# Kernel tuning notes

Measured on AMD Instinct MI355X. Metric: run time of the kernel, lower is better.

Reference implementation:

```python
import jax, jax.numpy as jnp
import numpy as np

B, N, S = 8, 8192, 2048
IN, SKIP, OUT, EXP = 256, 128, 256, 4
GROUPS = 8


def conv1d(x, w, b):
    # 1x1 conv: x [B,C,N], w [O,C], b [O]
    return jnp.einsum('bcn,oc->bon', x, w) + b[None, :, None]


def group_norm(x, w, b, groups=GROUPS, eps=1e-5):
    Bb, C, Nn = x.shape
    xg = x.reshape(Bb, groups, C // groups, Nn)
    m = xg.mean(axis=(2, 3), keepdims=True)
    v = xg.var(axis=(2, 3), keepdims=True)
    xn = ((xg - m) * jax.lax.rsqrt(v + eps)).reshape(Bb, C, Nn)
    return xn * w[None, :, None] + b[None, :, None]


def _forward(xyz1, points1, xyz2, points2, t_emb, c_emb,
             mlp_w, mlp_b, mlp_gw, mlp_gb,
             c1w, c1b, g1w, g1b, c2w, c2b, g2w, g2b,
             tw, tb, cw, cb):
    # pairwise squared distances [B,N,S]
    dists = (-2.0 * jnp.einsum('bcn,bcm->bnm', xyz1, xyz2)
             + jnp.sum(xyz1 ** 2, axis=1)[:, :, None]
             + jnp.sum(xyz2 ** 2, axis=1)[:, None, :])
    neg_d3, idx = jax.lax.top_k(-dists, 3)          # 3 smallest distances
    d3 = -neg_d3                                     # [B,N,3]
    recip = 1.0 / (d3 + 1e-8)
    weight = recip / jnp.sum(recip, axis=2, keepdims=True)
    # gather neighbor features: points2 [B,C,S], idx [B,N,3] -> [B,C,N,3]
    gathered = jax.vmap(lambda p, i: p[:, i])(points2, idx)
    interp = jnp.sum(gathered * weight[:, None, :, :], axis=3)  # [B,IN,N]

    new_points = jnp.concatenate([points1, interp], axis=1)     # [B,IN+SKIP,N]
    x = jax.nn.silu(group_norm(conv1d(new_points, mlp_w, mlp_b), mlp_gw, mlp_gb))

    identity = x
    h = jax.nn.silu(group_norm(conv1d(x, c1w, c1b), g1w, g1b))
    h = group_norm(conv1d(h, c2w, c2b), g2w, g2b)
    st = t_emb @ tw.T + tb
    sc = c_emb @ cw.T + cb
    scale_t, shift_t = jnp.split(st, 2, axis=1)
    scale_c, shift_c = jnp.split(sc, 2, axis=1)
    scale = (scale_t + scale_c)[:, :, None]
    shift = (shift_t + shift_c)[:, :, None]
    h = h * (1.0 + scale) + shift
    return h + identity


def setup_inputs() -> dict:
    key = jax.random.key(0)
    ks = jax.random.split(key, 12)
    def rn(k, shape, s=1.0):
        return jax.random.normal(k, shape, dtype=jnp.float32) * s
    E = OUT * EXP
    return dict(
        xyz1=rn(ks[0], (B, 3, N)),
        points1=rn(ks[1], (B, SKIP, N)),
        xyz2=rn(ks[2], (B, 3, S)),
        points2=rn(ks[3], (B, IN, S)),
        t_emb=rn(ks[4], (B, OUT)),
        c_emb=rn(ks[5], (B, OUT)),
        mlp_w=rn(ks[6], (OUT, IN + SKIP), 0.02), mlp_b=jnp.zeros((OUT,), jnp.float32),
        mlp_gw=jnp.ones((OUT,), jnp.float32), mlp_gb=jnp.zeros((OUT,), jnp.float32),
        c1w=rn(ks[7], (E, OUT), 0.02), c1b=jnp.zeros((E,), jnp.float32),
        g1w=jnp.ones((E,), jnp.float32), g1b=jnp.zeros((E,), jnp.float32),
        c2w=rn(ks[8], (OUT, E), 0.02), c2b=jnp.zeros((OUT,), jnp.float32),
        g2w=jnp.ones((OUT,), jnp.float32), g2b=jnp.zeros((OUT,), jnp.float32),
        tw=rn(ks[9], (2 * OUT, OUT), 0.02), tb=jnp.zeros((2 * OUT,), jnp.float32),
        cw=rn(ks[10], (2 * OUT, OUT), 0.02), cb=jnp.zeros((2 * OUT,), jnp.float32),
    )


def reference(xyz1, points1, xyz2, points2, t_emb, c_emb,
              mlp_w, mlp_b, mlp_gw, mlp_gb,
              c1w, c1b, g1w, g1b, c2w, c2b, g2w, g2b,
              tw, tb, cw, cb):
    return _forward(xyz1, points1, xyz2, points2, t_emb, c_emb,
                    mlp_w, mlp_b, mlp_gw, mlp_gb,
                    c1w, c1b, g1w, g1b, c2w, c2b, g2w, g2b,
                    tw, tb, cw, cb)
```

## Files before the change

kernel.cpp:

```cpp
#include <hip/hip_runtime.h>
#include <hip/hip_bf16.h>

typedef unsigned short u16;
typedef __attribute__((ext_vector_type(4))) float f32x4;
typedef __attribute__((ext_vector_type(8))) short bf16x8;

typedef const __attribute__((address_space(1))) void GV;
typedef __attribute__((address_space(3))) void LV;
#define GLOAD16(g, l) __builtin_amdgcn_global_load_lds((GV*)(g), (LV*)(l), 16, 0, 0)

__device__ __forceinline__ float b2f(u16 u) {
    union { float f; unsigned int i; } v; v.i = ((unsigned int)u) << 16; return v.f;
}
__device__ __forceinline__ u16 f2b(float f) {
    union { float f; unsigned int i; } v; v.f = f;
    unsigned int x = v.i;
    return (u16)((x + 0x7fffu + ((x >> 16) & 1u)) >> 16);
}
__device__ __forceinline__ unsigned int cvt_pk_bf16(float lo, float hi) {
    unsigned int d;
    asm("v_cvt_pk_bf16_f32 %0, %1, %2" : "=v"(d) : "v"(lo), "v"(hi));
    return d;
}
__device__ __forceinline__ float silu(float t) {
    return t * __builtin_amdgcn_rcpf(1.f + __expf(-t));
}

__global__ void knn_part_kernel(const float* __restrict__ xyz1, const float* __restrict__ xyz2,
                                float2* __restrict__ cand) {
    __shared__ float4 spt[256];
    int b = blockIdx.z, ck = blockIdx.y, tid = threadIdx.x;
    const float* p2 = xyz2 + (size_t)b * 3 * 2048;
    int s0 = ck << 8;
    {
        int s = s0 + tid;
        float x = p2[s], y = p2[2048 + s], z = p2[4096 + s];
        spt[tid] = make_float4(x, y, z, (x * x + y * y) + z * z);
    }
    __syncthreads();
    int n = blockIdx.x * 256 + tid;
    const float* p1 = xyz1 + (size_t)b * 3 * 8192;
    float qx = p1[n], qy = p1[8192 + n], qz = p1[16384 + n];
    float qn = (qx * qx + qy * qy) + qz * qz;
    float d0 = 3.4e38f, d1 = 3.4e38f, d2 = 3.4e38f;
    int i0 = 0, i1 = 0, i2 = 0;
#pragma unroll 4
    for (int s = 0; s < 256; ++s) {
        float4 p = spt[s];
        float dot = (qx * p.x + qy * p.y) + qz * p.z;
        float d = (-2.f * dot + qn) + p.w;
        if (d < d2) {
            int gi = s0 + s;
            if (d < d1) {
                if (d < d0) { d2 = d1; i2 = i1; d1 = d0; i1 = i0; d0 = d; i0 = gi; }
                else        { d2 = d1; i2 = i1; d1 = d;  i1 = gi; }
            } else          { d2 = d;  i2 = gi; }
        }
    }
    float2* c = cand + (((size_t)b * 8192 + n) * 8 + ck) * 3;
    c[0] = make_float2(d0, __int_as_float(i0));
    c[1] = make_float2(d1, __int_as_float(i1));
    c[2] = make_float2(d2, __int_as_float(i2));
}

__global__ void knn_merge_kernel(const float2* __restrict__ cand,
                                 int* __restrict__ idx_out, float* __restrict__ w_out) {
    int t = blockIdx.x * 256 + threadIdx.x;
    const float2* c = cand + (size_t)t * 24;
    float d0 = 3.4e38f, d1 = 3.4e38f, d2 = 3.4e38f;
    int i0 = 0, i1 = 0, i2 = 0;
#pragma unroll
    for (int k = 0; k < 24; ++k) {
        float2 p = c[k];
        float d = p.x;
        if (d < d2) {
            int gi = __float_as_int(p.y);
            if (d < d1) {
                if (d < d0) { d2 = d1; i2 = i1; d1 = d0; i1 = i0; d0 = d; i0 = gi; }
                else        { d2 = d1; i2 = i1; d1 = d;  i1 = gi; }
            } else          { d2 = d;  i2 = gi; }
        }
    }
    float r0 = 1.f / (d0 + 1e-8f), r1 = 1.f / (d1 + 1e-8f), r2 = 1.f / (d2 + 1e-8f);
    float inv = 1.f / (r0 + r1 + r2);
    size_t base = (size_t)t * 3;
    idx_out[base] = i0; idx_out[base + 1] = i1; idx_out[base + 2] = i2;
    w_out[base] = r0 * inv; w_out[base + 1] = r1 * inv; w_out[base + 2] = r2 * inv;
}

__global__ void tr_kernel(const float* __restrict__ src, u16* __restrict__ dst,
                          int C, int S, int dstStride) {
    __shared__ u16 tile[64][70];
    int b = blockIdx.z;
    int s0 = blockIdx.x * 64, c0 = blockIdx.y * 64;
    int tid = threadIdx.x, lane = tid & 63, wv = tid >> 6;
    const float* sp = src + ((size_t)b * C + c0) * S + s0;
    for (int c = wv; c < 64; c += 4)
        tile[lane][c] = f2b(sp[(size_t)c * S + lane]);
    __syncthreads();
    u16* dp = dst + ((size_t)b * S + s0) * dstStride + c0;
    int s = tid >> 5, cp = tid & 31;
#pragma unroll
    for (int k = 0; k < 8; ++k) {
        int r = s + k * 8;
        unsigned int v = *(const unsigned int*)&tile[r][cp * 2];
        *(unsigned int*)&dp[(size_t)r * dstStride + cp * 2] = v;
    }
}

__global__ void build_x0_kernel(const u16* __restrict__ p2t,
                                const int* __restrict__ idx, const float* __restrict__ wgt,
                                u16* __restrict__ x0t) {
    int b = blockIdx.y;
    int n = blockIdx.x * 64 + (threadIdx.x >> 2);
    int q = threadIdx.x & 3;
    size_t ib = ((size_t)b * 8192 + n) * 3;
    int j0 = idx[ib], j1 = idx[ib + 1], j2 = idx[ib + 2];
    float w0 = wgt[ib], w1 = wgt[ib + 1], w2 = wgt[ib + 2];
    const u16* r0 = p2t + ((size_t)b * 2048 + j0) * 256;
    const u16* r1 = p2t + ((size_t)b * 2048 + j1) * 256;
    const u16* r2 = p2t + ((size_t)b * 2048 + j2) * 256;
    u16* out = x0t + ((size_t)b * 8192 + n) * 384;
#pragma unroll
    for (int i = 0; i < 8; ++i) {
        int c = (i * 4 + q) * 8;
        bf16x8 a0 = *(const bf16x8*)&r0[c];
        bf16x8 a1 = *(const bf16x8*)&r1[c];
        bf16x8 a2 = *(const bf16x8*)&r2[c];
        u16 ovu[8] __attribute__((aligned(16)));
#pragma unroll
        for (int j = 0; j < 8; ++j) {
            float v = w0 * b2f((u16)a0[j]) + w1 * b2f((u16)a1[j]) + w2 * b2f((u16)a2[j]);
            ovu[j] = f2b(v);
        }
        *(uint4*)&out[128 + c] = *(const uint4*)ovu;
    }
}

__global__ void cvt_kernel(const float* __restrict__ src, u16* __restrict__ dst, int n) {
    int i = blockIdx.x * 256 + threadIdx.x;
    if (i < n) dst[i] = f2b(src[i]);
}

__global__ void film_kernel(const float* __restrict__ t_emb, const float* __restrict__ c_emb,
                            const float* __restrict__ tw, const float* __restrict__ tb,
                            const float* __restrict__ cw, const float* __restrict__ cb,
                            float* __restrict__ film) {
    __shared__ float te[256], ce[256];
    int b = blockIdx.x, tid = threadIdx.x;
    te[tid] = t_emb[b * 256 + tid];
    ce[tid] = c_emb[b * 256 + tid];
    __syncthreads();
    int j = tid + blockIdx.y * 256;
    const float* twr = tw + (size_t)j * 256;
    const float* cwr = cw + (size_t)j * 256;
    float s = 0.f;
    for (int k = 0; k < 256; ++k) s += te[k] * twr[k] + ce[k] * cwr[k];
    s += tb[j] + cb[j];
    film[b * 512 + j] = s;
}

__global__ __launch_bounds__(512, 4) void gemm_kernel(
        const u16* __restrict__ At, const u16* __restrict__ W, const float* __restrict__ bias,
        u16* __restrict__ Out, float* __restrict__ part,
        int K, int M, int gshift) {
    __shared__ u16 lA[2][128 * 64];
    __shared__ u16 lB[2][128 * 64];
    __shared__ float bpart[4][2];
    int b = blockIdx.z;
    int n0 = blockIdx.x * 128, o0 = blockIdx.y * 128;
    int tid = threadIdx.x, lane = tid & 63, wv = tid >> 6;
    int wn = wv & 1, wo = wv >> 1;
    if (tid < 8) ((float*)bpart)[tid] = 0.f;
    f32x4 acc[4][2];
#pragma unroll
    for (int i = 0; i < 4; i++)
#pragma unroll
        for (int j = 0; j < 2; j++) acc[i][j] = (f32x4){0.f, 0.f, 0.f, 0.f};

    int rl = lane >> 3;
    int csw = ((lane & 7) ^ rl) * 8;
    const u16* aP[2];
    const u16* bP[2];
#pragma unroll
    for (int p2 = 0; p2 < 2; p2++) {
        int p = wv * 2 + p2;
        aP[p2] = At + ((size_t)b * 8192 + n0 + p * 8 + rl) * K + csw;
        bP[p2] = W + ((size_t)(o0 + p * 8 + rl)) * K + csw;
    }
    int nK = K >> 6;
#pragma unroll
    for (int p2 = 0; p2 < 2; p2++) {
        int p = wv * 2 + p2;
        GLOAD16(aP[p2], &lA[0][p * 512]);
        GLOAD16(bP[p2], &lB[0][p * 512]);
        aP[p2] += 64; bP[p2] += 64;
    }
    asm volatile("s_waitcnt vmcnt(0) lgkmcnt(0)" ::: "memory");
    __builtin_amdgcn_s_barrier();
    int cur = 0;
    for (int kt = 0; kt < nK; ++kt) {
        if (kt + 1 < nK) {
#pragma unroll
            for (int p2 = 0; p2 < 2; p2++) {
                int p = wv * 2 + p2;
                GLOAD16(aP[p2], &lA[cur ^ 1][p * 512]);
                GLOAD16(bP[p2], &lB[cur ^ 1][p * 512]);
                aP[p2] += 64; bP[p2] += 64;
            }
        }
        const u16* la = lA[cur];
        const u16* lb = lB[cur];
#pragma unroll
        for (int kk = 0; kk < 2; kk++) {
            bf16x8 af[4], bfr[2];
#pragma unroll
            for (int mf = 0; mf < 4; mf++) {
                int R = wn * 64 + mf * 16 + (lane & 15);
                af[mf] = *(const bf16x8*)&la[R * 64 + ((kk * 4 + (lane >> 4)) ^ (R & 7)) * 8];
            }
#pragma unroll
            for (int nf = 0; nf < 2; nf++) {
                int R = wo * 32 + nf * 16 + (lane & 15);
                bfr[nf] = *(const bf16x8*)&lb[R * 64 + ((kk * 4 + (lane >> 4)) ^ (R & 7)) * 8];
            }
#pragma unroll
            for (int mf = 0; mf < 4; mf++)
#pragma unroll
                for (int nf = 0; nf < 2; nf++)
                    acc[mf][nf] = __builtin_amdgcn_mfma_f32_16x16x32_bf16(bfr[nf], af[mf], acc[mf][nf], 0, 0, 0);
        }
        if (kt + 1 < nK)
            asm volatile("s_waitcnt vmcnt(0)" ::: "memory");
        __builtin_amdgcn_s_barrier();
        cur ^= 1;
    }
    int oq = (lane >> 4) * 4;
    float4 bs[2];
    float s1[2] = {0.f, 0.f}, s2[2] = {0.f, 0.f};
#pragma unroll
    for (int nf = 0; nf < 2; nf++) bs[nf] = *(const float4*)&bias[o0 + wo * 32 + nf * 16 + oq];
#pragma unroll
    for (int mf = 0; mf < 4; mf++) {
        int n = n0 + wn * 64 + mf * 16 + (lane & 15);
        u16* rowp = Out + ((size_t)b * 8192 + n) * M + o0 + wo * 32 + oq;
#pragma unroll
        for (int nf = 0; nf < 2; nf++) {
            float v0 = acc[mf][nf][0] + bs[nf].x;
            float v1 = acc[mf][nf][1] + bs[nf].y;
            float v2 = acc[mf][nf][2] + bs[nf].z;
            float v3 = acc[mf][nf][3] + bs[nf].w;
            s1[nf] += (v0 + v1) + (v2 + v3);
            s2[nf] += (v0 * v0 + v1 * v1) + (v2 * v2 + v3 * v3);
            uint2 pk;
            pk.x = cvt_pk_bf16(v0, v1);
            pk.y = cvt_pk_bf16(v2, v3);
            *(uint2*)&rowp[nf * 16] = pk;
        }
    }
#pragma unroll
    for (int nf = 0; nf < 2; nf++) {
        float a = s1[nf], c = s2[nf];
#pragma unroll
        for (int off = 32; off > 0; off >>= 1) {
            a += __shfl_xor(a, off, 64);
            c += __shfl_xor(c, off, 64);
        }
        if (lane == 0) {
            int gl = (wo * 32 + nf * 16) >> gshift;
            atomicAdd(&bpart[gl][0], a);
            atomicAdd(&bpart[gl][1], c);
        }
    }
    __syncthreads();
    int nlg = 128 >> gshift;
    if (tid < 2 * nlg) {
        int gl = tid >> 1, s = tid & 1;
        int g = (o0 >> gshift) + gl;
        part[(((size_t)b * 8 + g) * 2 + s) * 64 + blockIdx.x] = bpart[gl][s];
    }
}

__global__ __launch_bounds__(512, 4) void gemm_gn_kernel(
        const u16* __restrict__ At, const u16* __restrict__ W, const float* __restrict__ bias,
        const float* __restrict__ tab,
        u16* __restrict__ Out, float* __restrict__ part,
        int K, int M, int gshift) {
    __shared__ u16 lA[2][128 * 64];
    __shared__ u16 lB[2][128 * 64];
    __shared__ float cA[1024], cB[1024];
    __shared__ float bpart[4][2];
    int b = blockIdx.z;
    int n0 = blockIdx.x * 128, o0 = blockIdx.y * 128;
    int tid = threadIdx.x, lane = tid & 63, wv = tid >> 6;
    int wn = wv & 1, wo = wv >> 1;
    if (tid < 8) ((float*)bpart)[tid] = 0.f;
    f32x4 acc[4][2];
#pragma unroll
    for (int i = 0; i < 4; i++)
#pragma unroll
        for (int j = 0; j < 2; j++) acc[i][j] = (f32x4){0.f, 0.f, 0.f, 0.f};

    int rl = lane >> 3;
    int csw = ((lane & 7) ^ rl) * 8;
    const u16* aP[2];
    const u16* bP[2];
#pragma unroll
    for (int p2 = 0; p2 < 2; p2++) {
        int p = wv * 2 + p2;
        aP[p2] = At + ((size_t)b * 8192 + n0 + p * 8 + rl) * K + csw;
        bP[p2] = W + ((size_t)(o0 + p * 8 + rl)) * K + csw;
    }
    int nK = K >> 6;
    uint4 areg[2];
#pragma unroll
    for (int p2 = 0; p2 < 2; p2++) { areg[p2] = *(const uint4*)aP[p2]; aP[p2] += 64; }
#pragma unroll
    for (int p2 = 0; p2 < 2; p2++) {
        int p = wv * 2 + p2;
        GLOAD16(bP[p2], &lB[0][p * 512]);
        bP[p2] += 64;
    }
    {
        const float* tA = tab + (size_t)b * K;
        const float* tB = tab + (size_t)(8 + b) * K;
        for (int i = tid; i < K; i += 512) { cA[i] = tA[i]; cB[i] = tB[i]; }
    }
    __syncthreads();
#pragma unroll
    for (int p2 = 0; p2 < 2; p2++) {
        int p = wv * 2 + p2;
        int c = csw;
        const u16* rr = (const u16*)&areg[p2];
        float4 a0 = *(const float4*)&cA[c], a1 = *(const float4*)&cA[c + 4];
        float4 b0 = *(const float4*)&cB[c], b1 = *(const float4*)&cB[c + 4];
        float va[8] = {a0.x, a0.y, a0.z, a0.w, a1.x, a1.y, a1.z, a1.w};
        float vb[8] = {b0.x, b0.y, b0.z, b0.w, b1.x, b1.y, b1.z, b1.w};
        float v[8];
#pragma unroll
        for (int j = 0; j < 8; ++j) v[j] = silu(b2f(rr[j]) * va[j] + vb[j]);
        uint4 o;
        o.x = cvt_pk_bf16(v[0], v[1]); o.y = cvt_pk_bf16(v[2], v[3]);
        o.z = cvt_pk_bf16(v[4], v[5]); o.w = cvt_pk_bf16(v[6], v[7]);
        *(uint4*)&lA[0][p * 512 + lane * 8] = o;
    }
    asm volatile("s_waitcnt vmcnt(0) lgkmcnt(0)" ::: "memory");
    __builtin_amdgcn_s_barrier();
    int cur = 0;
    for (int kt = 0; kt < nK; ++kt) {
        if (kt + 1 < nK) {
#pragma unroll
            for (int p2 = 0; p2 < 2; p2++) { areg[p2] = *(const uint4*)aP[p2]; aP[p2] += 64; }
#pragma unroll
            for (int p2 = 0; p2 < 2; p2++) {
                int p = wv * 2 + p2;
                GLOAD16(bP[p2], &lB[cur ^ 1][p * 512]);
                bP[p2] += 64;
            }
        }
        const u16* la = lA[cur];
        const u16* lb = lB[cur];
#pragma unroll
        for (int kk = 0; kk < 2; kk++) {
            bf16x8 af[4], bfr[2];
#pragma unroll
            for (int mf = 0; mf < 4; mf++) {
                int R = wn * 64 + mf * 16 + (lane & 15);
                af[mf] = *(const bf16x8*)&la[R * 64 + ((kk * 4 + (lane >> 4)) ^ (R & 7)) * 8];
            }
#pragma unroll
            for (int nf = 0; nf < 2; nf++) {
                int R = wo * 32 + nf * 16 + (lane & 15);
                bfr[nf] = *(const bf16x8*)&lb[R * 64 + ((kk * 4 + (lane >> 4)) ^ (R & 7)) * 8];
            }
#pragma unroll
            for (int mf = 0; mf < 4; mf++)
#pragma unroll
                for (int nf = 0; nf < 2; nf++)
                    acc[mf][nf] = __builtin_amdgcn_mfma_f32_16x16x32_bf16(bfr[nf], af[mf], acc[mf][nf], 0, 0, 0);
        }
        if (kt + 1 < nK) {
            int c = (kt + 1) * 64 + csw;
            float4 a0 = *(const float4*)&cA[c], a1 = *(const float4*)&cA[c + 4];
            float4 b0 = *(const float4*)&cB[c], b1 = *(const float4*)&cB[c + 4];
            float va[8] = {a0.x, a0.y, a0.z, a0.w, a1.x, a1.y, a1.z, a1.w};
            float vb[8] = {b0.x, b0.y, b0.z, b0.w, b1.x, b1.y, b1.z, b1.w};
#pragma unroll
            for (int p2 = 0; p2 < 2; p2++) {
                int p = wv * 2 + p2;
                const u16* rr = (const u16*)&areg[p2];
                float v[8];
#pragma unroll
                for (int j = 0; j < 8; ++j) v[j] = silu(b2f(rr[j]) * va[j] + vb[j]);
                uint4 o;
                o.x = cvt_pk_bf16(v[0], v[1]); o.y = cvt_pk_bf16(v[2], v[3]);
                o.z = cvt_pk_bf16(v[4], v[5]); o.w = cvt_pk_bf16(v[6], v[7]);
                *(uint4*)&lA[cur ^ 1][p * 512 + lane * 8] = o;
            }
            asm volatile("s_waitcnt vmcnt(0)" ::: "memory");
        }
        asm volatile("s_waitcnt lgkmcnt(0)" ::: "memory");
        __builtin_amdgcn_s_barrier();
        cur ^= 1;
    }
    int oq = (lane >> 4) * 4;
    float4 bs[2];
    float s1[2] = {0.f, 0.f}, s2[2] = {0.f, 0.f};
#pragma unroll
    for (int nf = 0; nf < 2; nf++) bs[nf] = *(const float4*)&bias[o0 + wo * 32 + nf * 16 + oq];
#pragma unroll
    for (int mf = 0; mf < 4; mf++) {
        int n = n0 + wn * 64 + mf * 16 + (lane & 15);
        u16* rowp = Out + ((size_t)b * 8192 + n) * M + o0 + wo * 32 + oq;
#pragma unroll
        for (int nf = 0; nf < 2; nf++) {
            float v0 = acc[mf][nf][0] + bs[nf].x;
            float v1 = acc[mf][nf][1] + bs[nf].y;
            float v2 = acc[mf][nf][2] + bs[nf].z;
            float v3 = acc[mf][nf][3] + bs[nf].w;
            s1[nf] += (v0 + v1) + (v2 + v3);
            s2[nf] += (v0 * v0 + v1 * v1) + (v2 * v2 + v3 * v3);
            uint2 pk;
            pk.x = cvt_pk_bf16(v0, v1);
            pk.y = cvt_pk_bf16(v2, v3);
            *(uint2*)&rowp[nf * 16] = pk;
        }
    }
#pragma unroll
    for (int nf = 0; nf < 2; nf++) {
        float a = s1[nf], c = s2[nf];
#pragma unroll
        for (int off = 32; off > 0; off >>= 1) {
            a += __shfl_xor(a, off, 64);
            c += __shfl_xor(c, off, 64);
        }
        if (lane == 0) {
            int gl = (wo * 32 + nf * 16) >> gshift;
            atomicAdd(&bpart[gl][0], a);
            atomicAdd(&bpart[gl][1], c);
        }
    }
    __syncthreads();
    int nlg = 128 >> gshift;
    if (tid < 2 * nlg) {
        int gl = tid >> 1, s = tid & 1;
        int g = (o0 >> gshift) + gl;
        part[(((size_t)b * 8 + g) * 2 + s) * 64 + blockIdx.x] = bpart[gl][s];
    }
}

__global__ void gn_reduce_kernel(const float* __restrict__ part, float* __restrict__ stats) {
    int t = threadIdx.x;
    const float4* p = (const float4*)(part + (size_t)t * 64);
    float s = 0.f;
#pragma unroll
    for (int i = 0; i < 16; i++) { float4 v = p[i]; s += (v.x + v.y) + (v.z + v.w); }
    stats[t] = s;
}

__global__ void gn_coef_kernel(const float* __restrict__ stats, const float* __restrict__ gw,
                               const float* __restrict__ gb, float* __restrict__ tab,
                               int K, int gshift, float invCnt) {
    int c = blockIdx.x * 256 + threadIdx.x;
    int b = blockIdx.y;
    int g = c >> gshift;
    float sum = stats[(b * 8 + g) * 2], ssq = stats[(b * 8 + g) * 2 + 1];
    float m = sum * invCnt;
    float rstd = rsqrtf(fmaxf(ssq * invCnt - m * m, 0.f) + 1e-5f);
    float A = rstd * gw[c];
    tab[(size_t)b * K + c] = A;
    tab[(size_t)(8 + b) * K + c] = gb[c] - m * A;
}

__global__ void gn_apply_kernel(const u16* __restrict__ Yin, u16* __restrict__ Yout,
                                const float* __restrict__ tab) {
    int t = blockIdx.x * 256 + threadIdx.x;
    int c8 = t & 31, c0 = c8 << 3;
    int row0 = t >> 5;
    int rowstep = (gridDim.x * 256) >> 5;
    float A[8], Bc[8];
    int bprev = -1;
    for (int row = row0; row < 65536; row += rowstep) {
        int b = row >> 13;
        if (b != bprev) {
            bprev = b;
            float4 a0 = *(const float4*)(tab + (size_t)b * 256 + c0);
            float4 a1 = *(const float4*)(tab + (size_t)b * 256 + c0 + 4);
            float4 b0 = *(const float4*)(tab + (size_t)(8 + b) * 256 + c0);
            float4 b1 = *(const float4*)(tab + (size_t)(8 + b) * 256 + c0 + 4);
            A[0]=a0.x;A[1]=a0.y;A[2]=a0.z;A[3]=a0.w;A[4]=a1.x;A[5]=a1.y;A[6]=a1.z;A[7]=a1.w;
            Bc[0]=b0.x;Bc[1]=b0.y;Bc[2]=b0.z;Bc[3]=b0.w;Bc[4]=b1.x;Bc[5]=b1.y;Bc[6]=b1.z;Bc[7]=b1.w;
        }
        size_t off = ((size_t)row << 8) + c0;
        uint4 v4 = *(const uint4*)(Yin + off);
        const u16* vu = (const u16*)&v4;
        float v[8];
#pragma unroll
        for (int j = 0; j < 8; j++) v[j] = silu(b2f(vu[j]) * A[j] + Bc[j]);
        uint4 o;
        o.x = cvt_pk_bf16(v[0], v[1]); o.y = cvt_pk_bf16(v[2], v[3]);
        o.z = cvt_pk_bf16(v[4], v[5]); o.w = cvt_pk_bf16(v[6], v[7]);
        *(uint4*)(Yout + off) = o;
    }
}

__global__ void final_kernel(const u16* __restrict__ Y2, const u16* __restrict__ Xraw,
                             const float* __restrict__ g0w, const float* __restrict__ g0b,
                             const float* __restrict__ stats0,
                             const float* __restrict__ g2w, const float* __restrict__ g2b,
                             const float* __restrict__ stats2, const float* __restrict__ film,
                             float* __restrict__ out) {
    __shared__ float tile[64][257];
    int b = blockIdx.y, n0 = blockIdx.x * 64, tid = threadIdx.x;
    const float invCnt = 1.f / (32.f * 8192.f);
    int c8 = tid & 31, c0 = c8 << 3, g = c8 >> 2;
    float sum = stats2[(b * 8 + g) * 2], ssq = stats2[(b * 8 + g) * 2 + 1];
    float m = sum * invCnt, rstd = rsqrtf(fmaxf(ssq * invCnt - m * m, 0.f) + 1e-5f);
    float sum0 = stats0[(b * 8 + g) * 2], ssq0 = stats0[(b * 8 + g) * 2 + 1];
    float m0 = sum0 * invCnt, rstd0 = rsqrtf(fmaxf(ssq0 * invCnt - m0 * m0, 0.f) + 1e-5f);
    float4 w0 = *(const float4*)(g2w + c0), w1 = *(const float4*)(g2w + c0 + 4);
    float4 q0 = *(const float4*)(g2b + c0), q1 = *(const float4*)(g2b + c0 + 4);
    float4 f0 = *(const float4*)(film + b * 512 + c0), f1 = *(const float4*)(film + b * 512 + c0 + 4);
    float4 h0 = *(const float4*)(film + b * 512 + 256 + c0), h1 = *(const float4*)(film + b * 512 + 256 + c0 + 4);
    float4 u0 = *(const float4*)(g0w + c0), u1 = *(const float4*)(g0w + c0 + 4);
    float4 e0 = *(const float4*)(g0b + c0), e1 = *(const float4*)(g0b + c0 + 4);
    float wv[8] = {w0.x, w0.y, w0.z, w0.w, w1.x, w1.y, w1.z, w1.w};
    float qv[8] = {q0.x, q0.y, q0.z, q0.w, q1.x, q1.y, q1.z, q1.w};
    float fs[8] = {f0.x, f0.y, f0.z, f0.w, f1.x, f1.y, f1.z, f1.w};
    float fh[8] = {h0.x, h0.y, h0.z, h0.w, h1.x, h1.y, h1.z, h1.w};
    float uv[8] = {u0.x, u0.y, u0.z, u0.w, u1.x, u1.y, u1.z, u1.w};
    float ev[8] = {e0.x, e0.y, e0.z, e0.w, e1.x, e1.y, e1.z, e1.w};
    float A[8], Bc[8], A0[8], B0[8];
#pragma unroll
    for (int j = 0; j < 8; j++) {
        float sc = 1.f + fs[j];
        A[j] = rstd * wv[j] * sc;
        Bc[j] = (qv[j] - m * rstd * wv[j]) * sc + fh[j];
        A0[j] = rstd0 * uv[j];
        B0[j] = ev[j] - m0 * A0[j];
    }
    int nrb = tid >> 5;
#pragma unroll
    for (int k = 0; k < 8; k++) {
        int nr = nrb + k * 8;
        size_t base = ((size_t)b * 8192 + n0 + nr) * 256 + c0;
        uint4 yv = *(const uint4*)(Y2 + base);
        uint4 xv = *(const uint4*)(Xraw + base);
        const u16* yy = (const u16*)&yv;
        const u16* xx = (const u16*)&xv;
#pragma unroll
        for (int j = 0; j < 8; j++) {
            float x = silu(b2f(xx[j]) * A0[j] + B0[j]);
            tile[nr][c0 + j] = b2f(yy[j]) * A[j] + Bc[j] + x;
        }
    }
    __syncthreads();
    for (int q = tid; q < 256 * 16; q += 256) {
        int c = q >> 4, n4 = q & 15;
        float4 o;
        o.x = tile[n4 * 4 + 0][c];
        o.y = tile[n4 * 4 + 1][c];
        o.z = tile[n4 * 4 + 2][c];
        o.w = tile[n4 * 4 + 3][c];
        *(float4*)&out[((size_t)b * 256 + c) * 8192 + n0 + n4 * 4] = o;
    }
}

extern "C" void kernel_launch(void* const* d_in, const int* in_sizes, int n_in,
                              void* d_out, int out_size, void* d_ws, size_t ws_size,
                              hipStream_t stream) {
    const float* xyz1    = (const float*)d_in[0];
    const float* points1 = (const float*)d_in[1];
    const float* xyz2    = (const float*)d_in[2];
    const float* points2 = (const float*)d_in[3];
    const float* t_emb   = (const float*)d_in[4];
    const float* c_emb   = (const float*)d_in[5];
    const float* mlp_w   = (const float*)d_in[6];
    const float* mlp_b   = (const float*)d_in[7];
    const float* mlp_gw  = (const float*)d_in[8];
    const float* mlp_gb  = (const float*)d_in[9];
    const float* c1w     = (const float*)d_in[10];
    const float* c1b     = (const float*)d_in[11];
    const float* g1w     = (const float*)d_in[12];
    const float* g1b     = (const float*)d_in[13];
    const float* c2w     = (const float*)d_in[14];
    const float* c2b     = (const float*)d_in[15];
    const float* g2w     = (const float*)d_in[16];
    const float* g2b     = (const float*)d_in[17];
    const float* tw      = (const float*)d_in[18];
    const float* tb      = (const float*)d_in[19];
    const float* cw      = (const float*)d_in[20];
    const float* cb      = (const float*)d_in[21];

    char* ws = (char*)d_ws;
    int*   idx    = (int*)ws;
    float* wgt    = (float*)(ws + 786432);
    float* stats0 = (float*)(ws + 1572864);
    float* stats1 = (float*)(ws + 1573376);
    float* stats2 = (float*)(ws + 1573888);
    float* film   = (float*)(ws + 1574400);
    float* part0  = (float*)(ws + 1590784);
    float* part1  = (float*)(ws + 1623552);
    float* part2  = (float*)(ws + 1656320);
    u16* wb_mlp   = (u16*)(ws + 1689088);
    u16* wb_c1    = (u16*)(ws + 1885696);
    u16* wb_c2    = (u16*)(ws + 2409984);
    float* tab0   = (float*)(ws + 2934272);
    float* tab1   = (float*)(ws + 2950656);
    u16* X0t = (u16*)(ws + 4194304);
    u16* Y1t = (u16*)(ws + 54525952);
    u16* H1t = (u16*)(ws + 88080384);
    u16* Y2t = X0t;
    u16* Y1act = X0t;
    float2* cand = (float2*)X0t;
    u16* p2t = H1t;
    float* out = (float*)d_out;

    cvt_kernel<<<384, 256, 0, stream>>>(mlp_w, wb_mlp, 98304);
    cvt_kernel<<<1024, 256, 0, stream>>>(c1w, wb_c1, 262144);
    cvt_kernel<<<1024, 256, 0, stream>>>(c2w, wb_c2, 262144);
    knn_part_kernel<<<dim3(32, 8, 8), 256, 0, stream>>>(xyz1, xyz2, cand);
    knn_merge_kernel<<<256, 256, 0, stream>>>(cand, idx, wgt);
    tr_kernel<<<dim3(128, 2, 8), 256, 0, stream>>>(points1, X0t, 128, 8192, 384);
    tr_kernel<<<dim3(32, 4, 8), 256, 0, stream>>>(points2, p2t, 256, 2048, 256);
    build_x0_kernel<<<dim3(128, 8), 256, 0, stream>>>(p2t, idx, wgt, X0t);
    film_kernel<<<dim3(8, 2), 256, 0, stream>>>(t_emb, c_emb, tw, tb, cw, cb, film);
    gemm_kernel<<<dim3(64, 2, 8), 512, 0, stream>>>(X0t, wb_mlp, mlp_b, Y1t, part0, 384, 256, 5);
    gn_reduce_kernel<<<1, 128, 0, stream>>>(part0, stats0);
    gn_coef_kernel<<<dim3(1, 8), 256, 0, stream>>>(stats0, mlp_gw, mlp_gb, tab0, 256, 5, 1.f / (32.f * 8192.f));
    gn_apply_kernel<<<512, 256, 0, stream>>>(Y1t, Y1act, tab0);
    gemm_kernel<<<dim3(64, 8, 8), 512, 0, stream>>>(Y1act, wb_c1, c1b, H1t, part1, 256, 1024, 7);
    gn_reduce_kernel<<<1, 128, 0, stream>>>(part1, stats1);
    gn_coef_kernel<<<dim3(4, 8), 256, 0, stream>>>(stats1, g1w, g1b, tab1, 1024, 7, 1.f / (128.f * 8192.f));
    gemm_gn_kernel<<<dim3(64, 2, 8), 512, 0, stream>>>(H1t, wb_c2, c2b, tab1, Y2t, part2, 1024, 256, 5);
    gn_reduce_kernel<<<1, 128, 0, stream>>>(part2, stats2);
    final_kernel<<<dim3(128, 8), 256, 0, stream>>>(Y2t, Y1t, mlp_gw, mlp_gb, stats0,
                                                   g2w, g2b, stats2, film, out);
}
```

Measured before the change: 360.0 us.

## Halve GEMM K-tile to 32, fuse weight conversions and GN stats/coef kernels

```diff
diff --git a/kernel.cpp b/kernel.cpp
--- a/kernel.cpp
+++ b/kernel.cpp
@@ -137,9 +137,13 @@
     }
 }
 
-__global__ void cvt_kernel(const float* __restrict__ src, u16* __restrict__ dst, int n) {
+__global__ void cvt3_kernel(const float* __restrict__ s0, u16* __restrict__ d0, int n0,
+                            const float* __restrict__ s1, u16* __restrict__ d1, int n1,
+                            const float* __restrict__ s2, u16* __restrict__ d2, int n2) {
     int i = blockIdx.x * 256 + threadIdx.x;
-    if (i < n) dst[i] = f2b(src[i]);
+    if (i < n0) d0[i] = f2b(s0[i]);
+    if (i < n1) d1[i] = f2b(s1[i]);
+    if (i < n2) d2[i] = f2b(s2[i]);
 }
 
 __global__ void film_kernel(const float* __restrict__ t_emb, const float* __restrict__ c_emb,
@@ -164,8 +168,8 @@
         const u16* __restrict__ At, const u16* __restrict__ W, const float* __restrict__ bias,
         u16* __restrict__ Out, float* __restrict__ part,
         int K, int M, int gshift) {
-    __shared__ u16 lA[2][128 * 64];
-    __shared__ u16 lB[2][128 * 64];
+    __shared__ u16 lA[2][128 * 32];
+    __shared__ u16 lB[2][128 * 32];
     __shared__ float bpart[4][2];
     int b = blockIdx.z;
     int n0 = blockIdx.x * 128, o0 = blockIdx.y * 128;
@@ -178,58 +182,42 @@
 #pragma unroll
         for (int j = 0; j < 2; j++) acc[i][j] = (f32x4){0.f, 0.f, 0.f, 0.f};
 
-    int rl = lane >> 3;
-    int csw = ((lane & 7) ^ rl) * 8;
-    const u16* aP[2];
-    const u16* bP[2];
-#pragma unroll
-    for (int p2 = 0; p2 < 2; p2++) {
-        int p = wv * 2 + p2;
-        aP[p2] = At + ((size_t)b * 8192 + n0 + p * 8 + rl) * K + csw;
-        bP[p2] = W + ((size_t)(o0 + p * 8 + rl)) * K + csw;
-    }
-    int nK = K >> 6;
-#pragma unroll
-    for (int p2 = 0; p2 < 2; p2++) {
-        int p = wv * 2 + p2;
-        GLOAD16(aP[p2], &lA[0][p * 512]);
-        GLOAD16(bP[p2], &lB[0][p * 512]);
-        aP[p2] += 64; bP[p2] += 64;
-    }
+    int row = tid >> 2;
+    int csrc = ((tid & 3) ^ ((row >> 1) & 3)) * 8;
+    const u16* aP = At + ((size_t)b * 8192 + n0 + row) * K + csrc;
+    const u16* bP = W + ((size_t)(o0 + row)) * K + csrc;
+    int nK = K >> 5;
+    GLOAD16(aP, &lA[0][wv * 512]);
+    GLOAD16(bP, &lB[0][wv * 512]);
+    aP += 32; bP += 32;
     asm volatile("s_waitcnt vmcnt(0) lgkmcnt(0)" ::: "memory");
     __builtin_amdgcn_s_barrier();
     int cur = 0;
+    int cs = lane >> 4;
     for (int kt = 0; kt < nK; ++kt) {
         if (kt + 1 < nK) {
-#pragma unroll
-            for (int p2 = 0; p2 < 2; p2++) {
-                int p = wv * 2 + p2;
-                GLOAD16(aP[p2], &lA[cur ^ 1][p * 512]);
-                GLOAD16(bP[p2], &lB[cur ^ 1][p * 512]);
-                aP[p2] += 64; bP[p2] += 64;
-            }
+            GLOAD16(aP, &lA[cur ^ 1][wv * 512]);
+            GLOAD16(bP, &lB[cur ^ 1][wv * 512]);
+            aP += 32; bP += 32;
         }
         const u16* la = lA[cur];
         const u16* lb = lB[cur];
-#pragma unroll
-        for (int kk = 0; kk < 2; kk++) {
-            bf16x8 af[4], bfr[2];
-#pragma unroll
-            for (int mf = 0; mf < 4; mf++) {
-                int R = wn * 64 + mf * 16 + (lane & 15);
-                af[mf] = *(const bf16x8*)&la[R * 64 + ((kk * 4 + (lane >> 4)) ^ (R & 7)) * 8];
-            }
-#pragma unroll
-            for (int nf = 0; nf < 2; nf++) {
-                int R = wo * 32 + nf * 16 + (lane & 15);
-                bfr[nf] = *(const bf16x8*)&lb[R * 64 + ((kk * 4 + (lane >> 4)) ^ (R & 7)) * 8];
-            }
-#pragma unroll
-            for (int mf = 0; mf < 4; mf++)
-#pragma unroll
-                for (int nf = 0; nf < 2; nf++)
-                    acc[mf][nf] = __builtin_amdgcn_mfma_f32_16x16x32_bf16(bfr[nf], af[mf], acc[mf][nf], 0, 0, 0);
-        }
+        bf16x8 af[4], bfr[2];
+#pragma unroll
+        for (int mf = 0; mf < 4; mf++) {
+            int R = wn * 64 + mf * 16 + (lane & 15);
+            af[mf] = *(const bf16x8*)&la[R * 32 + ((cs ^ ((R >> 1) & 3)) * 8)];
+        }
+#pragma unroll
+        for (int nf = 0; nf < 2; nf++) {
+            int R = wo * 32 + nf * 16 + (lane & 15);
+            bfr[nf] = *(const bf16x8*)&lb[R * 32 + ((cs ^ ((R >> 1) & 3)) * 8)];
+        }
+#pragma unroll
+        for (int mf = 0; mf < 4; mf++)
+#pragma unroll
+            for (int nf = 0; nf < 2; nf++)
+                acc[mf][nf] = __builtin_amdgcn_mfma_f32_16x16x32_bf16(bfr[nf], af[mf], acc[mf][nf], 0, 0, 0);
         if (kt + 1 < nK)
             asm volatile("s_waitcnt vmcnt(0)" ::: "memory");
         __builtin_amdgcn_s_barrier();
@@ -286,8 +274,8 @@
         const float* __restrict__ tab,
         u16* __restrict__ Out, float* __restrict__ part,
         int K, int M, int gshift) {
-    __shared__ u16 lA[2][128 * 64];
-    __shared__ u16 lB[2][128 * 64];
+    __shared__ u16 lA[2][128 * 32];
+    __shared__ u16 lB[2][128 * 32];
     __shared__ float cA[1024], cB[1024];
     __shared__ float bpart[4][2];
     int b = blockIdx.z;
@@ -301,37 +289,22 @@
 #pragma unroll
         for (int j = 0; j < 2; j++) acc[i][j] = (f32x4){0.f, 0.f, 0.f, 0.f};
 
-    int rl = lane >> 3;
-    int csw = ((lane & 7) ^ rl) * 8;
-    const u16* aP[2];
-    const u16* bP[2];
-#pragma unroll
-    for (int p2 = 0; p2 < 2; p2++) {
-        int p = wv * 2 + p2;
-        aP[p2] = At + ((size_t)b * 8192 + n0 + p * 8 + rl) * K + csw;
-        bP[p2] = W + ((size_t)(o0 + p * 8 + rl)) * K + csw;
-    }
-    int nK = K >> 6;
-    uint4 areg[2];
-#pragma unroll
-    for (int p2 = 0; p2 < 2; p2++) { areg[p2] = *(const uint4*)aP[p2]; aP[p2] += 64; }
-#pragma unroll
-    for (int p2 = 0; p2 < 2; p2++) {
-        int p = wv * 2 + p2;
-        GLOAD16(bP[p2], &lB[0][p * 512]);
-        bP[p2] += 64;
-    }
+    int row = tid >> 2;
+    int csrc = ((tid & 3) ^ ((row >> 1) & 3)) * 8;
+    const u16* aP = At + ((size_t)b * 8192 + n0 + row) * K + csrc;
+    const u16* bP = W + ((size_t)(o0 + row)) * K + csrc;
+    int nK = K >> 5;
+    uint4 areg = *(const uint4*)aP; aP += 32;
+    GLOAD16(bP, &lB[0][wv * 512]); bP += 32;
     {
         const float* tA = tab + (size_t)b * K;
         const float* tB = tab + (size_t)(8 + b) * K;
         for (int i = tid; i < K; i += 512) { cA[i] = tA[i]; cB[i] = tB[i]; }
     }
     __syncthreads();
-#pragma unroll
-    for (int p2 = 0; p2 < 2; p2++) {
-        int p = wv * 2 + p2;
-        int c = csw;
-        const u16* rr = (const u16*)&areg[p2];
+    {
+        int c = csrc;
+        const u16* rr = (const u16*)&areg;
         float4 a0 = *(const float4*)&cA[c], a1 = *(const float4*)&cA[c + 4];
         float4 b0 = *(const float4*)&cB[c], b1 = *(const float4*)&cB[c + 4];
         float va[8] = {a0.x, a0.y, a0.z, a0.w, a1.x, a1.y, a1.z, a1.w};
@@ -342,61 +315,49 @@
         uint4 o;
         o.x = cvt_pk_bf16(v[0], v[1]); o.y = cvt_pk_bf16(v[2], v[3]);
         o.z = cvt_pk_bf16(v[4], v[5]); o.w = cvt_pk_bf16(v[6], v[7]);
-        *(uint4*)&lA[0][p * 512 + lane * 8] = o;
+        *(uint4*)&lA[0][tid * 8] = o;
     }
     asm volatile("s_waitcnt vmcnt(0) lgkmcnt(0)" ::: "memory");
     __builtin_amdgcn_s_barrier();
     int cur = 0;
+    int cs = lane >> 4;
     for (int kt = 0; kt < nK; ++kt) {
         if (kt + 1 < nK) {
-#pragma unroll
-            for (int p2 = 0; p2 < 2; p2++) { areg[p2] = *(const uint4*)aP[p2]; aP[p2] += 64; }
-#pragma unroll
-            for (int p2 = 0; p2 < 2; p2++) {
-                int p = wv * 2 + p2;
-                GLOAD16(bP[p2], &lB[cur ^ 1][p * 512]);
-                bP[p2] += 64;
-            }
+            areg = *(const uint4*)aP; aP += 32;
+            GLOAD16(bP, &lB[cur ^ 1][wv * 512]); bP += 32;
         }
         const u16* la = lA[cur];
         const u16* lb = lB[cur];
-#pragma unroll
-        for (int kk = 0; kk < 2; kk++) {
-            bf16x8 af[4], bfr[2];
-#pragma unroll
-            for (int mf = 0; mf < 4; mf++) {
-                int R = wn * 64 + mf * 16 + (lane & 15);
-                af[mf] = *(const bf16x8*)&la[R * 64 + ((kk * 4 + (lane >> 4)) ^ (R & 7)) * 8];
-            }
-#pragma unroll
-            for (int nf = 0; nf < 2; nf++) {
-                int R = wo * 32 + nf * 16 + (lane & 15);
-                bfr[nf] = *(const bf16x8*)&lb[R * 64 + ((kk * 4 + (lane >> 4)) ^ (R & 7)) * 8];
-            }
-#pragma unroll
-            for (int mf = 0; mf < 4; mf++)
-#pragma unroll
-                for (int nf = 0; nf < 2; nf++)
-                    acc[mf][nf] = __builtin_amdgcn_mfma_f32_16x16x32_bf16(bfr[nf], af[mf], acc[mf][nf], 0, 0, 0);
-        }
+        bf16x8 af[4], bfr[2];
+#pragma unroll
+        for (int mf = 0; mf < 4; mf++) {
+            int R = wn * 64 + mf * 16 + (lane & 15);
+            af[mf] = *(const bf16x8*)&la[R * 32 + ((cs ^ ((R >> 1) & 3)) * 8)];
+        }
+#pragma unroll
+        for (int nf = 0; nf < 2; nf++) {
+            int R = wo * 32 + nf * 16 + (lane & 15);
+            bfr[nf] = *(const bf16x8*)&lb[R * 32 + ((cs ^ ((R >> 1) & 3)) * 8)];
+        }
+#pragma unroll
+        for (int mf = 0; mf < 4; mf++)
+#pragma unroll
+            for (int nf = 0; nf < 2; nf++)
+                acc[mf][nf] = __builtin_amdgcn_mfma_f32_16x16x32_bf16(bfr[nf], af[mf], acc[mf][nf], 0, 0, 0);
         if (kt + 1 < nK) {
-            int c = (kt + 1) * 64 + csw;
+            int c = (kt + 1) * 32 + csrc;
+            const u16* rr = (const u16*)&areg;
             float4 a0 = *(const float4*)&cA[c], a1 = *(const float4*)&cA[c + 4];
             float4 b0 = *(const float4*)&cB[c], b1 = *(const float4*)&cB[c + 4];
             float va[8] = {a0.x, a0.y, a0.z, a0.w, a1.x, a1.y, a1.z, a1.w};
             float vb[8] = {b0.x, b0.y, b0.z, b0.w, b1.x, b1.y, b1.z, b1.w};
-#pragma unroll
-            for (int p2 = 0; p2 < 2; p2++) {
-                int p = wv * 2 + p2;
-                const u16* rr = (const u16*)&areg[p2];
-                float v[8];
-#pragma unroll
-                for (int j = 0; j < 8; ++j) v[j] = silu(b2f(rr[j]) * va[j] + vb[j]);
-                uint4 o;
-                o.x = cvt_pk_bf16(v[0], v[1]); o.y = cvt_pk_bf16(v[2], v[3]);
-                o.z = cvt_pk_bf16(v[4], v[5]); o.w = cvt_pk_bf16(v[6], v[7]);
-                *(uint4*)&lA[cur ^ 1][p * 512 + lane * 8] = o;
-            }
+            float v[8];
+#pragma unroll
+            for (int j = 0; j < 8; ++j) v[j] = silu(b2f(rr[j]) * va[j] + vb[j]);
+            uint4 o;
+            o.x = cvt_pk_bf16(v[0], v[1]); o.y = cvt_pk_bf16(v[2], v[3]);
+            o.z = cvt_pk_bf16(v[4], v[5]); o.w = cvt_pk_bf16(v[6], v[7]);
+            *(uint4*)&lA[cur ^ 1][tid * 8] = o;
             asm volatile("s_waitcnt vmcnt(0)" ::: "memory");
         }
         asm volatile("s_waitcnt lgkmcnt(0)" ::: "memory");
@@ -449,27 +410,44 @@
     }
 }
 
-__global__ void gn_reduce_kernel(const float* __restrict__ part, float* __restrict__ stats) {
-    int t = threadIdx.x;
-    const float4* p = (const float4*)(part + (size_t)t * 64);
-    float s = 0.f;
-#pragma unroll
-    for (int i = 0; i < 16; i++) { float4 v = p[i]; s += (v.x + v.y) + (v.z + v.w); }
-    stats[t] = s;
-}
-
-__global__ void gn_coef_kernel(const float* __restrict__ stats, const float* __restrict__ gw,
-                               const float* __restrict__ gb, float* __restrict__ tab,
-                               int K, int gshift, float invCnt) {
-    int c = blockIdx.x * 256 + threadIdx.x;
-    int b = blockIdx.y;
-    int g = c >> gshift;
-    float sum = stats[(b * 8 + g) * 2], ssq = stats[(b * 8 + g) * 2 + 1];
+__global__ void gn_stats_coef_kernel(const float* __restrict__ part,
+                                     const float* __restrict__ gw, const float* __restrict__ gb,
+                                     float* __restrict__ stats, float* __restrict__ tab,
+                                     int K, int gshift, float invCnt) {
+    __shared__ float sg[16];
+    int b = blockIdx.y, c0 = blockIdx.x * 256, tid = threadIdx.x;
+    int ng = 256 >> gshift;
+    if (tid < 2 * ng) {
+        int gl = tid >> 1, s = tid & 1;
+        int g = (c0 >> gshift) + gl;
+        const float* p = part + (((size_t)b * 8 + g) * 2 + s) * 64;
+        float sum = 0.f;
+#pragma unroll
+        for (int i = 0; i < 64; i += 4) {
+            float4 v = *(const float4*)&p[i];
+            sum += (v.x + v.y) + (v.z + v.w);
+        }
+        sg[gl * 2 + s] = sum;
+        stats[((size_t)b * 8 + g) * 2 + s] = sum;
+    }
+    __syncthreads();
+    int c = c0 + tid;
+    int gl = tid >> gshift;
+    float sum = sg[gl * 2], ssq = sg[gl * 2 + 1];
     float m = sum * invCnt;
     float rstd = rsqrtf(fmaxf(ssq * invCnt - m * m, 0.f) + 1e-5f);
     float A = rstd * gw[c];
     tab[(size_t)b * K + c] = A;
     tab[(size_t)(8 + b) * K + c] = gb[c] - m * A;
+}
+
+__global__ void gn_reduce_kernel(const float* __restrict__ part, float* __restrict__ stats) {
+    int t = threadIdx.x;
+    const float4* p = (const float4*)(part + (size_t)t * 64);
+    float s = 0.f;
+#pragma unroll
+    for (int i = 0; i < 16; i++) { float4 v = p[i]; s += (v.x + v.y) + (v.z + v.w); }
+    stats[t] = s;
 }
 
 __global__ void gn_apply_kernel(const u16* __restrict__ Yin, u16* __restrict__ Yout,
@@ -616,9 +594,8 @@
     u16* p2t = H1t;
     float* out = (float*)d_out;
 
-    cvt_kernel<<<384, 256, 0, stream>>>(mlp_w, wb_mlp, 98304);
-    cvt_kernel<<<1024, 256, 0, stream>>>(c1w, wb_c1, 262144);
-    cvt_kernel<<<1024, 256, 0, stream>>>(c2w, wb_c2, 262144);
+    cvt3_kernel<<<1024, 256, 0, stream>>>(mlp_w, wb_mlp, 98304,
+                                          c1w, wb_c1, 262144, c2w, wb_c2, 262144);
     knn_part_kernel<<<dim3(32, 8, 8), 256, 0, stream>>>(xyz1, xyz2, cand);
     knn_merge_kernel<<<256, 256, 0, stream>>>(cand, idx, wgt);
     tr_kernel<<<dim3(128, 2, 8), 256, 0, stream>>>(points1, X0t, 128, 8192, 384);
@@ -626,12 +603,12 @@
     build_x0_kernel<<<dim3(128, 8), 256, 0, stream>>>(p2t, idx, wgt, X0t);
     film_kernel<<<dim3(8, 2), 256, 0, stream>>>(t_emb, c_emb, tw, tb, cw, cb, film);
     gemm_kernel<<<dim3(64, 2, 8), 512, 0, stream>>>(X0t, wb_mlp, mlp_b, Y1t, part0, 384, 256, 5);
-    gn_reduce_kernel<<<1, 128, 0, stream>>>(part0, stats0);
-    gn_coef_kernel<<<dim3(1, 8), 256, 0, stream>>>(stats0, mlp_gw, mlp_gb, tab0, 256, 5, 1.f / (32.f * 8192.f));
+    gn_stats_coef_kernel<<<dim3(1, 8), 256, 0, stream>>>(part0, mlp_gw, mlp_gb, stats0, tab0,
+                                                         256, 5, 1.f / (32.f * 8192.f));
     gn_apply_kernel<<<512, 256, 0, stream>>>(Y1t, Y1act, tab0);
     gemm_kernel<<<dim3(64, 8, 8), 512, 0, stream>>>(Y1act, wb_c1, c1b, H1t, part1, 256, 1024, 7);
-    gn_reduce_kernel<<<1, 128, 0, stream>>>(part1, stats1);
-    gn_coef_kernel<<<dim3(4, 8), 256, 0, stream>>>(stats1, g1w, g1b, tab1, 1024, 7, 1.f / (128.f * 8192.f));
+    gn_stats_coef_kernel<<<dim3(4, 8), 256, 0, stream>>>(part1, g1w, g1b, stats1, tab1,
+                                                         1024, 7, 1.f / (128.f * 8192.f));
     gemm_gn_kernel<<<dim3(64, 2, 8), 512, 0, stream>>>(H1t, wb_c2, c2b, tab1, Y2t, part2, 1024, 256, 5);
     gn_reduce_kernel<<<1, 128, 0, stream>>>(part2, stats2);
     final_kernel<<<dim3(128, 8), 256, 0, stream>>>(Y2t, Y1t, mlp_gw, mlp_gb, stats0,
```

Measured after the change: 349.0 us. -3.1%, faster.
